# Performance work log

Measured on AMD Instinct MI355X. Metric: run time of the kernel, lower is better.

## Reference

```python
import jax, jax.numpy as jnp
import numpy as np

BN_EPS = 1e-5
NEG_SLOPE = 0.2


def _bn(h, gamma, beta, axes):
    # training-mode batch norm over given axes; channels on last axis
    mu = jnp.mean(h, axis=axes, keepdims=True)
    var = jnp.var(h, axis=axes, keepdims=True)
    return (h - mu) * jax.lax.rsqrt(var + BN_EPS) * gamma + beta


def _leaky(h):
    return jnp.where(h >= 0, h, NEG_SLOPE * h)


def setup_inputs() -> dict:
    key = jax.random.key(0)
    k0, k1, k2, k3 = jax.random.split(key, 4)
    B, N, C, K, M = 8, 1024, 512, 20, 64  # M = dim // downrate
    x = jax.random.normal(k0, (B, N, C), dtype=jnp.float32)
    idx = jax.random.randint(k1, (B, N, K), 0, N, dtype=jnp.int32)
    W1 = jax.random.normal(k2, (M, 2 * C), dtype=jnp.float32) * (1.0 / np.sqrt(2 * C))
    gamma1 = jnp.ones((M,), jnp.float32)
    beta1 = jnp.zeros((M,), jnp.float32)
    W2 = jax.random.normal(k3, (C, M), dtype=jnp.float32) * (1.0 / np.sqrt(M))
    gamma2 = jnp.ones((C,), jnp.float32)
    beta2 = jnp.zeros((C,), jnp.float32)
    return dict(x=x, idx=idx, W1=W1, gamma1=gamma1, beta1=beta1,
                W2=W2, gamma2=gamma2, beta2=beta2)


def reference(x, idx, W1, gamma1, beta1, W2, gamma2, beta2):
    # x: (B, N, C) point features; idx: (B, N, K) neighbor indices into N
    neigh = jax.vmap(lambda xb, ib: xb[ib])(x, idx)          # (B, N, K, C) gather
    center = x[:, :, None, :]                                 # (B, N, 1, C)
    # get_graph_feature: concat(feature - x, x) -> channels = 2C
    edge = jnp.concatenate(
        [neigh - center, jnp.broadcast_to(center, neigh.shape)], axis=-1)  # (B,N,K,2C)
    # conv1: 1x1 conv == per-edge linear, then BN2d (stats over B,N,K) + LeakyReLU
    h = jnp.einsum('bnkc,mc->bnkm', edge, W1)                 # (B, N, K, M)
    h = _leaky(_bn(h, gamma1, beta1, (0, 1, 2)))
    # max-aggregate over neighbors
    h = jnp.max(h, axis=2)                                    # (B, N, M)
    # conv2: 1x1 conv1d, BN1d (stats over B,N) + LeakyReLU
    h2 = jnp.einsum('bnm,dm->bnd', h, W2)                     # (B, N, C)
    h2 = _leaky(_bn(h2, gamma2, beta2, (0, 1)))
    return h2  # (B, N, dim), matches final permute(0, 2, 1)
```

## Files before the change

### kernel.cpp

```cpp
#include <hip/hip_runtime.h>
#include <math.h>

#define B_ 8
#define N_ 1024
#define C_ 512
#define K_ 20
#define M_ 64
#define R_ (B_*N_)

typedef short bf16x8 __attribute__((ext_vector_type(8)));
typedef float f32x4  __attribute__((ext_vector_type(4)));

#define WS_Y     0
#define WS_HMM   (WS_Y + R_*64)
#define WS_P1A   (WS_HMM + R_*64)
#define WS_P2A   (WS_P1A + 128)
#define WS_HB    (WS_P2A + 1024)

__device__ __forceinline__ uint f2b(float f) {
    union { float f; uint u; } v; v.f = f;
    return (v.u + 0x7fffu + ((v.u >> 16) & 1u)) >> 16;
}
__device__ __forceinline__ uint2 f4_to_b4(float4 v) {
    uint2 r;
    r.x = f2b(v.x) | (f2b(v.y) << 16);
    r.y = f2b(v.z) | (f2b(v.w) << 16);
    return r;
}
__device__ __forceinline__ float bits2f(uint u) {
    union { uint u; float f; } v; v.u = u; return v.f;
}
__device__ __forceinline__ float lrelu(float v) { return v >= 0.f ? v : 0.2f * v; }

__global__ __launch_bounds__(512) void k_yz(const float* __restrict__ x,
                                            const float* __restrict__ W1,
                                            ushort* __restrict__ Y,
                                            float* __restrict__ P1a,
                                            float* __restrict__ P2a) {
    __shared__ __align__(16) char sW[2 * 16384];
    const int t = threadIdx.x, lane = t & 63, w = t >> 6;
    const int wr = w >> 2, wc = w & 3;
    const int r0 = blockIdx.x * 32;

    if (blockIdx.x == 0 && t < 128) P1a[t] = 0.f;
    if (blockIdx.x >= 1 && blockIdx.x <= 2) P2a[(blockIdx.x - 1) * 512 + t] = 0.f;

    int srow[2], sslot[2];
    size_t swsrc[2];
    int sdst[2];
#pragma unroll
    for (int q = 0; q < 2; ++q) {
        const int f = q * 512 + t;
        const int row = f >> 3, slot = f & 7;
        srow[q] = row; sslot[q] = slot;
        swsrc[q] = (row < 64 ? (size_t)row * 1024 : (size_t)(row - 64) * 1024 + 512)
                 + slot * 8;
        sdst[q] = row * 128 + ((slot * 16) ^ ((row & 7) << 4));
    }

    const int arow = r0 + wr * 16 + (lane & 15);
    const size_t xrow = (size_t)arow * 512;
    const int kb = (lane >> 4) * 8;

    int boff[2][2];
#pragma unroll
    for (int g = 0; g < 2; ++g)
#pragma unroll
        for (int jj = 0; jj < 2; ++jj) {
            const int jrow = wc * 32 + jj * 16 + (lane & 15);
            boff[g][jj] = jrow * 128 + ((g * 64 + (lane >> 4) * 16) ^ ((jrow & 7) << 4));
        }

    float4 sA[2][2], sN[2][2];
#pragma unroll
    for (int q = 0; q < 2; ++q) {
        sA[q][0] = *(const float4*)&W1[swsrc[q]];
        sA[q][1] = *(const float4*)&W1[swsrc[q] + 4];
    }
    float4 xa[4], xn[4];
    xa[0] = *(const float4*)&x[xrow + kb];
    xa[1] = *(const float4*)&x[xrow + kb + 4];
    xa[2] = *(const float4*)&x[xrow + 32 + kb];
    xa[3] = *(const float4*)&x[xrow + 32 + kb + 4];

#pragma unroll
    for (int q = 0; q < 2; ++q) {
        const uint2 lo = f4_to_b4(sA[q][0]), hi = f4_to_b4(sA[q][1]);
        uint4 v; v.x = lo.x; v.y = lo.y; v.z = hi.x; v.w = hi.y;
        *(uint4*)(sW + sdst[q]) = v;
    }
    __syncthreads();

    f32x4 acc[2];
    acc[0] = (f32x4){0.f, 0.f, 0.f, 0.f};
    acc[1] = (f32x4){0.f, 0.f, 0.f, 0.f};

    for (int ks = 0; ks < 8; ++ks) {
        const int cur = ks & 1;
        const char* buf = sW + cur * 16384;

        if (ks < 7) {
            const int k0 = (ks + 1) * 64;
#pragma unroll
            for (int q = 0; q < 2; ++q) {
                sN[q][0] = *(const float4*)&W1[swsrc[q] + k0];
                sN[q][1] = *(const float4*)&W1[swsrc[q] + k0 + 4];
            }
            xn[0] = *(const float4*)&x[xrow + k0 + kb];
            xn[1] = *(const float4*)&x[xrow + k0 + kb + 4];
            xn[2] = *(const float4*)&x[xrow + k0 + 32 + kb];
            xn[3] = *(const float4*)&x[xrow + k0 + 32 + kb + 4];
        }

#pragma unroll
        for (int g = 0; g < 2; ++g) {
            const uint2 c0 = f4_to_b4(xa[g * 2]), c1 = f4_to_b4(xa[g * 2 + 1]);
            union { uint4 u; bf16x8 b; } A;
            A.u.x = c0.x; A.u.y = c0.y; A.u.z = c1.x; A.u.w = c1.y;
#pragma unroll
            for (int jj = 0; jj < 2; ++jj) {
                const bf16x8 Bf = *(const bf16x8*)(buf + boff[g][jj]);
                acc[jj] = __builtin_amdgcn_mfma_f32_16x16x32_bf16(A.b, Bf, acc[jj], 0, 0, 0);
            }
        }

        if (ks < 7) {
            char* nbuf = sW + (cur ^ 1) * 16384;
#pragma unroll
            for (int q = 0; q < 2; ++q) {
                const uint2 lo = f4_to_b4(sN[q][0]), hi = f4_to_b4(sN[q][1]);
                uint4 v; v.x = lo.x; v.y = lo.y; v.z = hi.x; v.w = hi.y;
                *(uint4*)(nbuf + sdst[q]) = v;
            }
#pragma unroll
            for (int i = 0; i < 4; ++i) xa[i] = xn[i];
        }
        __syncthreads();
    }

    const int crow = r0 + wr * 16 + (lane >> 4) * 4;
    const int ccol = wc * 32 + (lane & 15);
#pragma unroll
    for (int jj = 0; jj < 2; ++jj)
#pragma unroll
        for (int i = 0; i < 4; ++i)
            Y[(size_t)(crow + i) * 128 + ccol + jj * 16] = (ushort)f2b(acc[jj][i]);
}

__global__ __launch_bounds__(256) void k_gather(const ushort* __restrict__ Y,
                                                const int* __restrict__ idx,
                                                uint* __restrict__ HMM,
                                                float* __restrict__ P1a) {
    __shared__ float sSum[8][64];
    __shared__ float sQ[8][64];
    const int t = threadIdx.x, lane = t & 63, w = t >> 6;
    const int sub = lane >> 5, c = lane & 31;
    const int grp = w * 2 + sub;
    const uint* Yu = (const uint*)Y;
    float sum0 = 0.f, sum1 = 0.f, sq0 = 0.f, sq1 = 0.f;

#pragma unroll
    for (int pi = 0; pi < 4; ++pi) {
        const int p = blockIdx.x * 32 + w * 8 + pi * 2 + sub;
        const int bb = p >> 10;
        const uint ysu = Yu[(size_t)p * 64 + c];
        const uint zsu = Yu[(size_t)p * 64 + 32 + c];
        const float base0 = bits2f(zsu << 16) - bits2f(ysu << 16);
        const float base1 = bits2f(zsu & 0xffff0000u) - bits2f(ysu & 0xffff0000u);
        float mx0 = -INFINITY, mx1 = -INFINITY, mn0 = INFINITY, mn1 = INFINITY;
        int4 j4[5];
#pragma unroll
        for (int q = 0; q < 5; ++q) j4[q] = *(const int4*)&idx[p * 20 + q * 4];
#pragma unroll
        for (int k = 0; k < 20; ++k) {
            const int j = ((const int*)j4)[k];
            const uint yg = Yu[(size_t)(bb * 1024 + j) * 64 + c];
            const float h0 = bits2f(yg << 16) + base0;
            const float h1 = bits2f(yg & 0xffff0000u) + base1;
            sum0 += h0; sum1 += h1;
            sq0 += h0 * h0; sq1 += h1 * h1;
            mx0 = fmaxf(mx0, h0); mx1 = fmaxf(mx1, h1);
            mn0 = fminf(mn0, h0); mn1 = fminf(mn1, h1);
        }
        uint2 st;
        st.x = f2b(mx0) | (f2b(mn0) << 16);
        st.y = f2b(mx1) | (f2b(mn1) << 16);
        *(uint2*)&HMM[(size_t)p * 64 + 2 * c] = st;
    }

    *(float2*)&sSum[grp][2 * c] = make_float2(sum0, sum1);
    *(float2*)&sQ[grp][2 * c]   = make_float2(sq0, sq1);
    __syncthreads();
    if (t < 64) {
        float s = 0.f, q = 0.f;
#pragma unroll
        for (int g = 0; g < 8; ++g) { s += sSum[g][t]; q += sQ[g][t]; }
        atomicAdd(&P1a[t], s);
        atomicAdd(&P1a[64 + t], q);
    }
}

__global__ __launch_bounds__(256) void k_qsum(const uint* __restrict__ HMM,
                                              const float* __restrict__ P1a,
                                              const float* __restrict__ g1,
                                              const float* __restrict__ b1,
                                              const float* __restrict__ W2,
                                              ushort* __restrict__ Hb,
                                              float* __restrict__ P2a) {
    __shared__ float sSc1[64], sSh1[64];
    const int t = threadIdx.x, lane = t & 63, w = t >> 6;
    if (t < 64) {
        const float inv = 1.f / (float)(R_ * K_);
        const float mu  = P1a[t] * inv;
        const float var = P1a[64 + t] * inv - mu * mu;
        const float rs  = rsqrtf(var + 1e-5f);
        const float sc  = g1[t] * rs;
        sSc1[t] = sc;
        sSh1[t] = b1[t] - mu * sc;
    }
    __syncthreads();

    const int rtile = blockIdx.x, half = blockIdx.y;
    const int r0 = rtile * 64;
    const int dsub = half * 256 + w * 64;
    const int qd = lane >> 4, s = lane & 15;
    const int mc0 = qd * 8;

    bf16x8 bfr[4][2];
#pragma unroll
    for (int f = 0; f < 4; ++f) {
        const int d = dsub + f * 16 + s;
#pragma unroll
        for (int g = 0; g < 2; ++g) {
            const float4 wa = *(const float4*)&W2[(size_t)d * 64 + mc0 + g * 32];
            const float4 wb = *(const float4*)&W2[(size_t)d * 64 + mc0 + g * 32 + 4];
            const uint2 lo = f4_to_b4(wa), hi = f4_to_b4(wb);
            union { uint4 u; bf16x8 b; } cv;
            cv.u.x = lo.x; cv.u.y = lo.y; cv.u.z = hi.x; cv.u.w = hi.y;
            bfr[f][g] = cv.b;
        }
    }

    f32x4 acc[4][4];
#pragma unroll
    for (int rt = 0; rt < 4; ++rt)
#pragma unroll
        for (int f = 0; f < 4; ++f) acc[rt][f] = (f32x4){0.f,0.f,0.f,0.f};

#pragma unroll
    for (int rt = 0; rt < 4; ++rt) {
        const int row = r0 + rt * 16 + s;
#pragma unroll
        for (int g = 0; g < 2; ++g) {
            const int mc = mc0 + g * 32;
            const uint4 u0 = *(const uint4*)&HMM[(size_t)row * 64 + mc];
            const uint4 u1 = *(const uint4*)&HMM[(size_t)row * 64 + mc + 4];
            float v[8];
#pragma unroll
            for (int i = 0; i < 4; ++i) {
                const uint ua = ((const uint*)&u0)[i];
                const uint ub = ((const uint*)&u1)[i];
                const float c0 = sSc1[mc + i],     h0 = sSh1[mc + i];
                const float c4 = sSc1[mc + 4 + i], h4 = sSh1[mc + 4 + i];
                const float a0 = c0 >= 0.f ? bits2f(ua << 16) : bits2f(ua & 0xffff0000u);
                const float a4 = c4 >= 0.f ? bits2f(ub << 16) : bits2f(ub & 0xffff0000u);
                v[i]     = lrelu(a0 * c0 + h0);
                v[i + 4] = lrelu(a4 * c4 + h4);
            }
            uint4 pk;
            pk.x = f2b(v[0]) | (f2b(v[1]) << 16);
            pk.y = f2b(v[2]) | (f2b(v[3]) << 16);
            pk.z = f2b(v[4]) | (f2b(v[5]) << 16);
            pk.w = f2b(v[6]) | (f2b(v[7]) << 16);
            if (half == 0) *(uint4*)&Hb[(size_t)row * 64 + mc] = pk;
            union { uint4 u; bf16x8 b; } cv; cv.u = pk;
#pragma unroll
            for (int f = 0; f < 4; ++f)
                acc[rt][f] = __builtin_amdgcn_mfma_f32_16x16x32_bf16(cv.b, bfr[f][g], acc[rt][f], 0, 0, 0);
        }
    }

#pragma unroll
    for (int f = 0; f < 4; ++f) {
        float ss = 0.f, qq = 0.f;
#pragma unroll
        for (int rt = 0; rt < 4; ++rt)
#pragma unroll
            for (int i = 0; i < 4; ++i) {
                const float vv = acc[rt][f][i];
                ss += vv; qq += vv * vv;
            }
        ss += __shfl_xor(ss, 16); ss += __shfl_xor(ss, 32);
        qq += __shfl_xor(qq, 16); qq += __shfl_xor(qq, 32);
        if (lane < 16) {
            const int d = dsub + f * 16 + s;
            atomicAdd(&P2a[d], ss);
            atomicAdd(&P2a[512 + d], qq);
        }
    }
}

__global__ __launch_bounds__(256) void k_out(const ushort* __restrict__ Hb,
                                             const float* __restrict__ W2,
                                             const float* __restrict__ P2a,
                                             const float* __restrict__ g2,
                                             const float* __restrict__ b2,
                                             float* __restrict__ out) {
    __shared__ float sSc2[256], sSh2[256];
    const int t = threadIdx.x, lane = t & 63, w = t >> 6;
    const int rtile = blockIdx.x, half = blockIdx.y;
    {
        const int d = half * 256 + t;
        const float inv = 1.f / (float)R_;
        const float mu  = P2a[d] * inv;
        const float var = P2a[512 + d] * inv - mu * mu;
        const float rs  = rsqrtf(var + 1e-5f);
        const float sc  = g2[d] * rs;
        sSc2[t] = sc;
        sSh2[t] = b2[d] - mu * sc;
    }
    __syncthreads();

    const int r0 = rtile * 64;
    const int dsub = half * 256 + w * 64;
    const int qd = lane >> 4, s = lane & 15;
    const int mc0 = qd * 8;

    bf16x8 bfr[4][2];
#pragma unroll
    for (int f = 0; f < 4; ++f) {
        const int d = dsub + f * 16 + s;
#pragma unroll
        for (int g = 0; g < 2; ++g) {
            const float4 wa = *(const float4*)&W2[(size_t)d * 64 + mc0 + g * 32];
            const float4 wb = *(const float4*)&W2[(size_t)d * 64 + mc0 + g * 32 + 4];
            const uint2 lo = f4_to_b4(wa), hi = f4_to_b4(wb);
            union { uint4 u; bf16x8 b; } cv;
            cv.u.x = lo.x; cv.u.y = lo.y; cv.u.z = hi.x; cv.u.w = hi.y;
            bfr[f][g] = cv.b;
        }
    }

    f32x4 acc[4][4];
#pragma unroll
    for (int rt = 0; rt < 4; ++rt)
#pragma unroll
        for (int f = 0; f < 4; ++f) acc[rt][f] = (f32x4){0.f,0.f,0.f,0.f};

#pragma unroll
    for (int rt = 0; rt < 4; ++rt) {
        const int row = r0 + rt * 16 + s;
#pragma unroll
        for (int g = 0; g < 2; ++g) {
            const bf16x8 af = *(const bf16x8*)&Hb[(size_t)row * 64 + mc0 + g * 32];
#pragma unroll
            for (int f = 0; f < 4; ++f)
                acc[rt][f] = __builtin_amdgcn_mfma_f32_16x16x32_bf16(af, bfr[f][g], acc[rt][f], 0, 0, 0);
        }
    }

#pragma unroll
    for (int rt = 0; rt < 4; ++rt)
#pragma unroll
        for (int f = 0; f < 4; ++f) {
            const int dl = w * 64 + f * 16 + s;
            const float c2 = sSc2[dl], h2 = sSh2[dl];
            const int d = dsub + f * 16 + s;
#pragma unroll
            for (int i = 0; i < 4; ++i) {
                const float vv = lrelu(acc[rt][f][i] * c2 + h2);
                out[(size_t)(r0 + rt * 16 + qd * 4 + i) * 512 + d] = vv;
            }
        }
}

extern "C" void kernel_launch(void* const* d_in, const int* in_sizes, int n_in,
                              void* d_out, int out_size, void* d_ws, size_t ws_size,
                              hipStream_t stream) {
    const float* x   = (const float*)d_in[0];
    const int*   idx = (const int*)d_in[1];
    const float* W1  = (const float*)d_in[2];
    const float* g1  = (const float*)d_in[3];
    const float* b1  = (const float*)d_in[4];
    const float* W2  = (const float*)d_in[5];
    const float* g2  = (const float*)d_in[6];
    const float* b2  = (const float*)d_in[7];
    float* out = (float*)d_out;
    float* ws  = (float*)d_ws;

    ushort* Y    = (ushort*)(ws + WS_Y);
    uint*   HMM  = (uint*)(ws + WS_HMM);
    float*  P1a  = ws + WS_P1A;
    float*  P2a  = ws + WS_P2A;
    ushort* Hb   = (ushort*)(ws + WS_HB);

    k_yz    <<<dim3(R_ / 32), dim3(512), 0, stream>>>(x, W1, Y, P1a, P2a);
    k_gather<<<dim3(R_ / 32), dim3(256), 0, stream>>>(Y, idx, HMM, P1a);
    k_qsum  <<<dim3(128, 2),  dim3(256), 0, stream>>>(HMM, P1a, g1, b1, W2, Hb, P2a);
    k_out   <<<dim3(128, 2),  dim3(256), 0, stream>>>(Hb, W2, P2a, g2, b2, out);
}
```

Before: 45.79 us.

## Fuse stats and output kernels with a grid-wide atomic barrier

Merges the conv2 statistics kernel and the output kernel into one launch. Each block keeps its conv2 accumulators in registers, waits at a software grid barrier (atomic counter spin) until all 256 blocks have contributed BN2 sums, then normalizes and writes the output directly. This removes a kernel launch, the Hb intermediate write and read, and the recomputation of the second GEMM. It relies on all 256 blocks being co-resident on the GPU; without that guarantee the spin could deadlock.

```diff
diff --git a/kernel.cpp b/kernel.cpp
--- a/kernel.cpp
+++ b/kernel.cpp
@@ -15,7 +15,7 @@
 #define WS_HMM   (WS_Y + R_*64)
 #define WS_P1A   (WS_HMM + R_*64)
 #define WS_P2A   (WS_P1A + 128)
-#define WS_HB    (WS_P2A + 1024)
+#define WS_BAR   (WS_P2A + 1024)
 
 __device__ __forceinline__ uint f2b(float f) {
     union { float f; uint u; } v; v.f = f;
@@ -36,7 +36,8 @@
                                             const float* __restrict__ W1,
                                             ushort* __restrict__ Y,
                                             float* __restrict__ P1a,
-                                            float* __restrict__ P2a) {
+                                            float* __restrict__ P2a,
+                                            uint* __restrict__ bar) {
     __shared__ __align__(16) char sW[2 * 16384];
     const int t = threadIdx.x, lane = t & 63, w = t >> 6;
     const int wr = w >> 2, wc = w & 3;
@@ -44,15 +45,14 @@
 
     if (blockIdx.x == 0 && t < 128) P1a[t] = 0.f;
     if (blockIdx.x >= 1 && blockIdx.x <= 2) P2a[(blockIdx.x - 1) * 512 + t] = 0.f;
-
-    int srow[2], sslot[2];
+    if (blockIdx.x == 3 && t == 0) bar[0] = 0u;
+
     size_t swsrc[2];
     int sdst[2];
 #pragma unroll
     for (int q = 0; q < 2; ++q) {
         const int f = q * 512 + t;
         const int row = f >> 3, slot = f & 7;
-        srow[q] = row; sslot[q] = slot;
         swsrc[q] = (row < 64 ? (size_t)row * 1024 : (size_t)(row - 64) * 1024 + 512)
                  + slot * 8;
         sdst[q] = row * 128 + ((slot * 16) ^ ((row & 7) << 4));
@@ -200,13 +200,16 @@
     }
 }
 
-__global__ __launch_bounds__(256) void k_qsum(const uint* __restrict__ HMM,
+__global__ __launch_bounds__(256) void k_fuse(const uint* __restrict__ HMM,
                                               const float* __restrict__ P1a,
                                               const float* __restrict__ g1,
                                               const float* __restrict__ b1,
                                               const float* __restrict__ W2,
-                                              ushort* __restrict__ Hb,
-                                              float* __restrict__ P2a) {
+                                              const float* __restrict__ g2,
+                                              const float* __restrict__ b2,
+                                              float* __restrict__ P2a,
+                                              uint* __restrict__ bar,
+                                              float* __restrict__ out) {
     __shared__ float sSc1[64], sSh1[64];
     const int t = threadIdx.x, lane = t & 63, w = t >> 6;
     if (t < 64) {
@@ -272,7 +275,6 @@
             pk.y = f2b(v[2]) | (f2b(v[3]) << 16);
             pk.z = f2b(v[4]) | (f2b(v[5]) << 16);
             pk.w = f2b(v[6]) | (f2b(v[7]) << 16);
-            if (half == 0) *(uint4*)&Hb[(size_t)row * 64 + mc] = pk;
             union { uint4 u; bf16x8 b; } cv; cv.u = pk;
 #pragma unroll
             for (int f = 0; f < 4; ++f)
@@ -298,77 +300,41 @@
             atomicAdd(&P2a[512 + d], qq);
         }
     }
-}
-
-__global__ __launch_bounds__(256) void k_out(const ushort* __restrict__ Hb,
-                                             const float* __restrict__ W2,
-                                             const float* __restrict__ P2a,
-                                             const float* __restrict__ g2,
-                                             const float* __restrict__ b2,
-                                             float* __restrict__ out) {
-    __shared__ float sSc2[256], sSh2[256];
-    const int t = threadIdx.x, lane = t & 63, w = t >> 6;
-    const int rtile = blockIdx.x, half = blockIdx.y;
-    {
-        const int d = half * 256 + t;
+
+    __threadfence();
+    __syncthreads();
+    if (t == 0) {
+        __hip_atomic_fetch_add(bar, 1u, __ATOMIC_ACQ_REL, __HIP_MEMORY_SCOPE_AGENT);
+        uint v = __hip_atomic_load(bar, __ATOMIC_ACQUIRE, __HIP_MEMORY_SCOPE_AGENT);
+        while (v < 256u) {
+            __builtin_amdgcn_s_sleep(8);
+            v = __hip_atomic_load(bar, __ATOMIC_ACQUIRE, __HIP_MEMORY_SCOPE_AGENT);
+        }
+    }
+    __syncthreads();
+
+    float c2[4], h2s[4];
+#pragma unroll
+    for (int f = 0; f < 4; ++f) {
+        const int d = dsub + f * 16 + s;
+        const float ps = __hip_atomic_load(&P2a[d],       __ATOMIC_RELAXED, __HIP_MEMORY_SCOPE_AGENT);
+        const float pq = __hip_atomic_load(&P2a[512 + d], __ATOMIC_RELAXED, __HIP_MEMORY_SCOPE_AGENT);
         const float inv = 1.f / (float)R_;
-        const float mu  = P2a[d] * inv;
-        const float var = P2a[512 + d] * inv - mu * mu;
+        const float mu  = ps * inv;
+        const float var = pq * inv - mu * mu;
         const float rs  = rsqrtf(var + 1e-5f);
         const float sc  = g2[d] * rs;
-        sSc2[t] = sc;
-        sSh2[t] = b2[d] - mu * sc;
-    }
-    __syncthreads();
-
-    const int r0 = rtile * 64;
-    const int dsub = half * 256 + w * 64;
-    const int qd = lane >> 4, s = lane & 15;
-    const int mc0 = qd * 8;
-
-    bf16x8 bfr[4][2];
-#pragma unroll
-    for (int f = 0; f < 4; ++f) {
-        const int d = dsub + f * 16 + s;
-#pragma unroll
-        for (int g = 0; g < 2; ++g) {
-            const float4 wa = *(const float4*)&W2[(size_t)d * 64 + mc0 + g * 32];
-            const float4 wb = *(const float4*)&W2[(size_t)d * 64 + mc0 + g * 32 + 4];
-            const uint2 lo = f4_to_b4(wa), hi = f4_to_b4(wb);
-            union { uint4 u; bf16x8 b; } cv;
-            cv.u.x = lo.x; cv.u.y = lo.y; cv.u.z = hi.x; cv.u.w = hi.y;
-            bfr[f][g] = cv.b;
-        }
-    }
-
-    f32x4 acc[4][4];
+        c2[f]  = sc;
+        h2s[f] = b2[d] - mu * sc;
+    }
 #pragma unroll
     for (int rt = 0; rt < 4; ++rt)
 #pragma unroll
-        for (int f = 0; f < 4; ++f) acc[rt][f] = (f32x4){0.f,0.f,0.f,0.f};
-
-#pragma unroll
-    for (int rt = 0; rt < 4; ++rt) {
-        const int row = r0 + rt * 16 + s;
-#pragma unroll
-        for (int g = 0; g < 2; ++g) {
-            const bf16x8 af = *(const bf16x8*)&Hb[(size_t)row * 64 + mc0 + g * 32];
-#pragma unroll
-            for (int f = 0; f < 4; ++f)
-                acc[rt][f] = __builtin_amdgcn_mfma_f32_16x16x32_bf16(af, bfr[f][g], acc[rt][f], 0, 0, 0);
-        }
-    }
-
-#pragma unroll
-    for (int rt = 0; rt < 4; ++rt)
-#pragma unroll
         for (int f = 0; f < 4; ++f) {
-            const int dl = w * 64 + f * 16 + s;
-            const float c2 = sSc2[dl], h2 = sSh2[dl];
             const int d = dsub + f * 16 + s;
 #pragma unroll
             for (int i = 0; i < 4; ++i) {
-                const float vv = lrelu(acc[rt][f][i] * c2 + h2);
+                const float vv = lrelu(acc[rt][f][i] * c2[f] + h2s[f]);
                 out[(size_t)(r0 + rt * 16 + qd * 4 + i) * 512 + d] = vv;
             }
         }
@@ -392,10 +358,9 @@
     uint*   HMM  = (uint*)(ws + WS_HMM);
     float*  P1a  = ws + WS_P1A;
     float*  P2a  = ws + WS_P2A;
-    ushort* Hb   = (ushort*)(ws + WS_HB);
-
-    k_yz    <<<dim3(R_ / 32), dim3(512), 0, stream>>>(x, W1, Y, P1a, P2a);
+    uint*   bar  = (uint*)(ws + WS_BAR);
+
+    k_yz    <<<dim3(R_ / 32), dim3(512), 0, stream>>>(x, W1, Y, P1a, P2a, bar);
     k_gather<<<dim3(R_ / 32), dim3(256), 0, stream>>>(Y, idx, HMM, P1a);
-    k_qsum  <<<dim3(128, 2),  dim3(256), 0, stream>>>(HMM, P1a, g1, b1, W2, Hb, P2a);
-    k_out   <<<dim3(128, 2),  dim3(256), 0, stream>>>(Hb, W2, P2a, g2, b2, out);
-}
+    k_fuse  <<<dim3(128, 2),  dim3(256), 0, stream>>>(HMM, P1a, g1, b1, W2, g2, b2, P2a, bar, out);
+}
```

After: 65.04 us. +42.1%, slower.
